# Performance work log

Hardware: AMD Instinct MI355X
Metric: run time of the kernel (lower is better)

## Reference

```python
import jax, jax.numpy as jnp
import numpy as np

B, S, H, V = 256, 64, 512, 32000


def setup_inputs() -> dict:
    key = jax.random.key(0)
    ks = jax.random.split(key, 26)
    f32 = jnp.float32

    def n(k, shape, scale):
        return jax.random.normal(k, shape, dtype=f32) * scale

    s_h = 1.0 / np.sqrt(H)        # torch LSTMCell init scale ~ U(-1/sqrt(H),1/sqrt(H)); use normal of same scale
    s_2h = 1.0 / np.sqrt(2 * H)
    kn_h = np.sqrt(2.0 / H)       # kaiming_normal std for (B,H) tensor (fan_in = H)
    kn_2h = np.sqrt(2.0 / (2 * H))

    inp = {}
    inp["x"] = jax.random.randint(ks[0], (B, S), 0, V)
    inp["W_emb"] = n(ks[1], (V, H), 1.0)
    # forward cell
    inp["Wih_f"] = n(ks[2], (4 * H, H), s_h)
    inp["Whh_f"] = n(ks[3], (4 * H, H), s_h)
    inp["bih_f"] = n(ks[4], (4 * H,), s_h)
    inp["bhh_f"] = n(ks[5], (4 * H,), s_h)
    # backward cell
    inp["Wih_b"] = n(ks[6], (4 * H, H), s_h)
    inp["Whh_b"] = n(ks[7], (4 * H, H), s_h)
    inp["bih_b"] = n(ks[8], (4 * H,), s_h)
    inp["bhh_b"] = n(ks[9], (4 * H,), s_h)
    # combiner cell (input 2H, hidden 2H)
    inp["Wih_c"] = n(ks[10], (8 * H, 2 * H), s_2h)
    inp["Whh_c"] = n(ks[11], (8 * H, 2 * H), s_2h)
    inp["bih_c"] = n(ks[12], (8 * H,), s_2h)
    inp["bhh_c"] = n(ks[13], (8 * H,), s_2h)
    # linear head
    inp["Wout"] = n(ks[14], (V, 2 * H), s_2h)
    inp["bout"] = n(ks[15], (V,), s_2h)
    # kaiming-normal initial states
    inp["h0f"] = n(ks[16], (B, H), kn_h)
    inp["c0f"] = n(ks[17], (B, H), kn_h)
    inp["h0b"] = n(ks[18], (B, H), kn_h)
    inp["c0b"] = n(ks[19], (B, H), kn_h)
    inp["h0c"] = n(ks[20], (B, 2 * H), kn_2h)
    inp["c0c"] = n(ks[21], (B, 2 * H), kn_2h)
    return inp


def run_lstm(xs, h0, c0, Wih, Whh, b):
    # xs: (S, B, D). PyTorch LSTMCell gate order: i, f, g, o.
    def step(carry, x_t):
        h, c = carry
        g = x_t @ Wih.T + h @ Whh.T + b
        i, f, gg, o = jnp.split(g, 4, axis=-1)
        i = jax.nn.sigmoid(i)
        f = jax.nn.sigmoid(f)
        gg = jnp.tanh(gg)
        o = jax.nn.sigmoid(o)
        c2 = f * c + i * gg
        h2 = o * jnp.tanh(c2)
        return (h2, c2), h2
    _, hs = jax.lax.scan(step, (h0, c0), xs)
    return hs  # (S, B, hidden)


def reference(x, W_emb, Wih_f, Whh_f, bih_f, bhh_f, Wih_b, Whh_b, bih_b, bhh_b,
              Wih_c, Whh_c, bih_c, bhh_c, Wout, bout, h0f, c0f, h0b, c0b, h0c, c0c):
    b_sz, s_len = x.shape
    W = W_emb.at[0].set(0.0)                 # padding_idx=0
    emb = W[x]                               # (B, S, H)
    seq = emb.reshape(s_len, b_sz, -1)       # faithful to original .view(S, B, -1) (raw reshape, not transpose)
    hf = run_lstm(seq, h0f, c0f, Wih_f, Whh_f, bih_f + bhh_f)            # (S, B, H)
    hb = run_lstm(seq[::-1], h0b, c0b, Wih_b, Whh_b, bih_b + bhh_b)      # (S, B, H), produced order
    comb_in = jnp.concatenate([hf, hb], axis=-1)                          # (S, B, 2H)
    hc = run_lstm(comb_in, h0c, c0c, Wih_c, Whh_c, bih_c + bhh_c)        # (S, B, 2H)
    return hc[-1] @ Wout.T + bout                                         # (B, V)
```

## Files before the change

kernel.cpp:

```cpp
#include <hip/hip_runtime.h>

#define BB 256
#define SS 64
#define HH 512
#define VV 32000

typedef unsigned short u16;
typedef __attribute__((ext_vector_type(8))) short bf16x8;
typedef __attribute__((ext_vector_type(4))) float f32x4;

__device__ __forceinline__ float sigm(float x) { return 1.0f / (1.0f + __expf(-x)); }
__device__ __forceinline__ float tanh_fast(float x) { return 1.0f - 2.0f / (__expf(2.0f * x) + 1.0f); }
__device__ __forceinline__ u16 f2bf(float f) {
    unsigned u = __float_as_uint(f);
    return (u16)((u + 0x7fffu + ((u >> 16) & 1u)) >> 16);
}
__device__ __forceinline__ bf16x8 ld_cvt8(const float* s) {
    float4 v0 = *(const float4*)s, v1 = *(const float4*)(s + 4);
    bf16x8 b;
    b[0] = (short)f2bf(v0.x); b[1] = (short)f2bf(v0.y);
    b[2] = (short)f2bf(v0.z); b[3] = (short)f2bf(v0.w);
    b[4] = (short)f2bf(v1.x); b[5] = (short)f2bf(v1.y);
    b[6] = (short)f2bf(v1.z); b[7] = (short)f2bf(v1.w);
    return b;
}

#define MFMA(a, b, c) __builtin_amdgcn_mfma_f32_16x16x32_bf16(a, b, c, 0, 0, 0)

__global__ __launch_bounds__(256)
void pack_k(const int* __restrict__ x, const float* __restrict__ W_emb,
            const float* __restrict__ Wih_f, const float* __restrict__ Whh_f,
            const float* __restrict__ Wih_b, const float* __restrict__ Whh_b,
            const float* __restrict__ Wih_c, const float* __restrict__ Whh_c,
            u16* __restrict__ Xfrag, u16* __restrict__ Wfsw,
            u16* __restrict__ Wbsw, u16* __restrict__ Wcsw)
{
    const int lane = threadIdx.x & 63;
    const int l15 = lane & 15, quad = lane >> 4;
    const int gw0 = blockIdx.x * 4 + (threadIdx.x >> 6);
    const int nw = gridDim.x * 4;
    for (int task = gw0; task < 40960; task += nw) {
        const float* src; u16* dst; float scale = 1.f;
        if (task < 16384) {
            int s = task >> 8, rem = task & 255, mt = rem >> 4, kc = rem & 15;
            int b = mt * 16 + l15;
            int tok = x[s * 256 + b];
            scale = (tok == 0) ? 0.f : 1.f;
            src = W_emb + (size_t)tok * 512 + kc * 32 + quad * 8;
            dst = Xfrag + ((size_t)(s * 16 + mt) * 16 + kc) * 512 + (size_t)lane * 8;
        } else if (task < 24576) {
            int e = task - 16384;
            int which = e >> 12; e &= 4095;
            int ut = e >> 7, rem = e & 127, kc = rem >> 2, g = rem & 3;
            int row = g * 512 + ut * 16 + l15;
            int k0 = kc * 32 + quad * 8;
            const float* Wih = which ? Wih_b : Wih_f;
            const float* Whh = which ? Whh_b : Whh_f;
            src = (k0 < 512) ? (Wih + (size_t)row * 512 + k0)
                             : (Whh + (size_t)row * 512 + (k0 - 512));
            u16* W = which ? Wbsw : Wfsw;
            dst = W + ((size_t)(ut * 32 + kc) * 4 + g) * 512 + (size_t)lane * 8;
        } else {
            int e = task - 24576;
            int ut = e >> 8, rem = e & 255, kc = rem >> 2, g = rem & 3;
            int row = g * 1024 + ut * 16 + l15;
            int k0 = kc * 32 + quad * 8;
            src = (k0 < 1024) ? (Wih_c + (size_t)row * 1024 + k0)
                              : (Whh_c + (size_t)row * 1024 + (k0 - 1024));
            dst = Wcsw + ((size_t)(ut * 64 + kc) * 4 + g) * 512 + (size_t)lane * 8;
        }
        float4 v0 = *(const float4*)src;
        float4 v1 = *(const float4*)(src + 4);
        bf16x8 o;
        o[0] = (short)f2bf(v0.x * scale); o[1] = (short)f2bf(v0.y * scale);
        o[2] = (short)f2bf(v0.z * scale); o[3] = (short)f2bf(v0.w * scale);
        o[4] = (short)f2bf(v1.x * scale); o[5] = (short)f2bf(v1.y * scale);
        o[6] = (short)f2bf(v1.z * scale); o[7] = (short)f2bf(v1.w * scale);
        *(bf16x8*)dst = o;
    }
}

__global__ __launch_bounds__(256)
void init_k(const float* __restrict__ bih_f, const float* __restrict__ bhh_f,
            const float* __restrict__ bih_b, const float* __restrict__ bhh_b,
            const float* __restrict__ bih_c, const float* __restrict__ bhh_c,
            const float* __restrict__ h0f, const float* __restrict__ c0f,
            const float* __restrict__ h0b, const float* __restrict__ c0b,
            const float* __restrict__ h0c, const float* __restrict__ c0c,
            float* __restrict__ bsf, float* __restrict__ bsb, float* __restrict__ bsc,
            u16* __restrict__ hf0, u16* __restrict__ hb0, u16* __restrict__ hc0,
            float* __restrict__ cf, float* __restrict__ cb, float* __restrict__ cc)
{
    const int gid = blockIdx.x * 256 + threadIdx.x;
    if (gid < 2048)       bsf[gid] = bih_f[gid] + bhh_f[gid];
    else if (gid < 4096)  { int e = gid - 2048; bsb[e] = bih_b[e] + bhh_b[e]; }
    else if (gid < 8192)  { int e = gid - 4096; bsc[e] = bih_c[e] + bhh_c[e]; }
    const int stride = gridDim.x * 256;
    for (int i = gid; i < 131072; i += stride) {
        int b = i >> 9, k = i & 511;
        int dst = ((b >> 4) * 16 + (k >> 5)) * 512 + (((b & 15) + (((k >> 3) & 3) << 4)) << 3) + (k & 7);
        hf0[dst] = f2bf(h0f[i]);
        hb0[dst] = f2bf(h0b[i]);
        cf[i] = c0f[i];
        cb[i] = c0b[i];
    }
    for (int i = gid; i < 262144; i += stride) {
        int b = i >> 10, k = i & 1023;
        int dst = ((b >> 4) * 32 + (k >> 5)) * 512 + (((b & 15) + (((k >> 3) & 3) << 4)) << 3) + (k & 7);
        hc0[dst] = f2bf(h0c[i]);
        cc[i] = c0c[i];
    }
}

__global__ __launch_bounds__(256)
void step_k(const u16* __restrict__ Xfrag,
            const u16* __restrict__ Wfsw, const u16* __restrict__ Wbsw,
            const u16* __restrict__ Wcsw,
            const float* __restrict__ bsf, const float* __restrict__ bsb,
            const float* __restrict__ bsc,
            const u16* __restrict__ hf_r, u16* __restrict__ hf_w, float* __restrict__ cf,
            const u16* __restrict__ hb_r, u16* __restrict__ hb_w, float* __restrict__ cb,
            const u16* __restrict__ hc_r, u16* __restrict__ hc_w, float* __restrict__ cc,
            int t)
{
    __shared__ __align__(16) u16 Bsh[2][2][4][512];
    const int tid = threadIdx.x;
    const int w = tid >> 6, lane = tid & 63;
    const int l15 = lane & 15, quad = lane >> 4;
    const int xcd = blockIdx.x & 7, slot = blockIdx.x >> 3;
    const f32x4 z = {0.f, 0.f, 0.f, 0.f};

    if (slot < 32) {
        if (t >= SS) return;
        const int cell = xcd >> 2;
        const int ut = (xcd & 3) * 8 + (slot >> 2);
        const int mq = slot & 3;
        const int mt = mq * 4 + w;
        const u16* Wsw = cell ? Wbsw : Wfsw;
        const float* bs = cell ? bsb : bsf;
        const u16* h_r = cell ? hb_r : hf_r;
        u16* h_w = cell ? hb_w : hf_w;
        float* c = cell ? cb : cf;
        const int s2 = cell ? (SS - 1 - t) : t;

        const u16* wstage = Wsw + (size_t)ut * 65536 + (size_t)w * 512 + (size_t)lane * 8;
        const u16* xb0 = Xfrag + ((size_t)(s2 * 16 + mt) * 16) * 512 + (size_t)lane * 8;
        const u16* hp0 = h_r + ((size_t)(mt * 16)) * 512 + (size_t)lane * 8;

        f32x4 acc[4];
#pragma unroll
        for (int g = 0; g < 4; ++g) acc[g] = z;

#define AFB(f) (((f) < 16) ? (xb0 + (size_t)(f) * 512) : (hp0 + (size_t)((f) - 16) * 512))
        bf16x8 a0[3], a1[3];
        {
            bf16x8 w00 = *(const bf16x8*)(wstage);
            bf16x8 w01 = *(const bf16x8*)(wstage + 2048);
            bf16x8 w10 = *(const bf16x8*)(wstage + 2 * 2048);
            bf16x8 w11 = *(const bf16x8*)(wstage + 3 * 2048);
            a0[0] = *(const bf16x8*)AFB(0); a1[0] = *(const bf16x8*)AFB(1);
            a0[1] = *(const bf16x8*)AFB(2); a1[1] = *(const bf16x8*)AFB(3);
            *(bf16x8*)&Bsh[0][0][w][(size_t)lane * 8] = w00;
            *(bf16x8*)&Bsh[0][1][w][(size_t)lane * 8] = w01;
            *(bf16x8*)&Bsh[1][0][w][(size_t)lane * 8] = w10;
            *(bf16x8*)&Bsh[1][1][w][(size_t)lane * 8] = w11;
            __syncthreads();
        }
#pragma unroll
        for (int p = 0; p < 16; ++p) {
            const int s = p % 3, sn = (p + 2) % 3, cur = p & 1;
            bf16x8 wr0, wr1;
            const bool pre = (p + 2 < 16);
            if (pre) {
                wr0 = *(const bf16x8*)(wstage + (size_t)(2 * p + 4) * 2048);
                wr1 = *(const bf16x8*)(wstage + (size_t)(2 * p + 5) * 2048);
                a0[sn] = *(const bf16x8*)AFB(2 * p + 4);
                a1[sn] = *(const bf16x8*)AFB(2 * p + 5);
            }
#pragma unroll
            for (int g = 0; g < 4; ++g) {
                bf16x8 b0 = *(const bf16x8*)&Bsh[cur][0][g][(size_t)lane * 8];
                bf16x8 b1 = *(const bf16x8*)&Bsh[cur][1][g][(size_t)lane * 8];
                acc[g] = MFMA(a0[s], b0, acc[g]);
                acc[g] = MFMA(a1[s], b1, acc[g]);
            }
            __syncthreads();
            if (pre) {
                *(bf16x8*)&Bsh[cur][0][w][(size_t)lane * 8] = wr0;
                *(bf16x8*)&Bsh[cur][1][w][(size_t)lane * 8] = wr1;
            }
        }
#undef AFB

        const int u = ut * 16 + l15;
        const float bi_ = bs[u], bf_ = bs[512 + u], bg_ = bs[1024 + u], bo_ = bs[1536 + u];
        const int fragk = ut >> 1;
        const int lanehi = ((ut & 1) * 2 + (l15 >> 3)) << 4;
        const int j = l15 & 7;
#pragma unroll
        for (int r = 0; r < 4; ++r) {
            const int b = mt * 16 + quad * 4 + r;
            const size_t ci = (size_t)b * 512 + u;
            float i_ = sigm(acc[0][r] + bi_);
            float f_ = sigm(acc[1][r] + bf_);
            float g_ = tanh_fast(acc[2][r] + bg_);
            float o_ = sigm(acc[3][r] + bo_);
            float c2 = f_ * c[ci] + i_ * g_;
            c[ci] = c2;
            h_w[(size_t)(mt * 16 + fragk) * 512 + (size_t)((quad * 4 + r) + lanehi) * 8 + j]
                = f2bf(o_ * tanh_fast(c2));
        }
    } else {
        if (t == 0) return;
        const int cs = slot - 32;
        const int ut = xcd * 8 + (cs >> 2);
        const int mq = cs & 3;
        const int mt = mq * 4 + w;

        const u16* wstage = Wcsw + (size_t)ut * 131072 + (size_t)w * 512 + (size_t)lane * 8;
        const u16* hfa = hf_r + ((size_t)(mt * 16)) * 512 + (size_t)lane * 8;
        const u16* hba = hb_r + ((size_t)(mt * 16)) * 512 + (size_t)lane * 8;
        const u16* hca = hc_r + ((size_t)(mt * 32)) * 512 + (size_t)lane * 8;

        f32x4 acc[4];
#pragma unroll
        for (int g = 0; g < 4; ++g) acc[g] = z;

#define ACB(f)  (((f) < 16) ? (hfa + (size_t)(f) * 512) \
               : ((f) < 32) ? (hba + (size_t)((f) - 16) * 512) \
                            : (hca + (size_t)((f) - 32) * 512))
        bf16x8 a0[3], a1[3];
        {
            bf16x8 w00 = *(const bf16x8*)(wstage);
            bf16x8 w01 = *(const bf16x8*)(wstage + 2048);
            bf16x8 w10 = *(const bf16x8*)(wstage + 2 * 2048);
            bf16x8 w11 = *(const bf16x8*)(wstage + 3 * 2048);
            a0[0] = *(const bf16x8*)ACB(0); a1[0] = *(const bf16x8*)ACB(1);
            a0[1] = *(const bf16x8*)ACB(2); a1[1] = *(const bf16x8*)ACB(3);
            *(bf16x8*)&Bsh[0][0][w][(size_t)lane * 8] = w00;
            *(bf16x8*)&Bsh[0][1][w][(size_t)lane * 8] = w01;
            *(bf16x8*)&Bsh[1][0][w][(size_t)lane * 8] = w10;
            *(bf16x8*)&Bsh[1][1][w][(size_t)lane * 8] = w11;
            __syncthreads();
        }
#pragma unroll
        for (int p = 0; p < 32; ++p) {
            const int s = p % 3, sn = (p + 2) % 3, cur = p & 1;
            bf16x8 wr0, wr1;
            const bool pre = (p + 2 < 32);
            if (pre) {
                wr0 = *(const bf16x8*)(wstage + (size_t)(2 * p + 4) * 2048);
                wr1 = *(const bf16x8*)(wstage + (size_t)(2 * p + 5) * 2048);
                a0[sn] = *(const bf16x8*)ACB(2 * p + 4);
                a1[sn] = *(const bf16x8*)ACB(2 * p + 5);
            }
#pragma unroll
            for (int g = 0; g < 4; ++g) {
                bf16x8 b0 = *(const bf16x8*)&Bsh[cur][0][g][(size_t)lane * 8];
                bf16x8 b1 = *(const bf16x8*)&Bsh[cur][1][g][(size_t)lane * 8];
                acc[g] = MFMA(a0[s], b0, acc[g]);
                acc[g] = MFMA(a1[s], b1, acc[g]);
            }
            __syncthreads();
            if (pre) {
                *(bf16x8*)&Bsh[cur][0][w][(size_t)lane * 8] = wr0;
                *(bf16x8*)&Bsh[cur][1][w][(size_t)lane * 8] = wr1;
            }
        }
#undef ACB

        const int u = ut * 16 + l15;
        const float bi_ = bsc[u], bf_ = bsc[1024 + u], bg_ = bsc[2048 + u], bo_ = bsc[3072 + u];
        const int fragk = ut >> 1;
        const int lanehi = ((ut & 1) * 2 + (l15 >> 3)) << 4;
        const int j = l15 & 7;
#pragma unroll
        for (int r = 0; r < 4; ++r) {
            const int b = mt * 16 + quad * 4 + r;
            const size_t ci = (size_t)b * 1024 + u;
            float i_ = sigm(acc[0][r] + bi_);
            float f_ = sigm(acc[1][r] + bf_);
            float g_ = tanh_fast(acc[2][r] + bg_);
            float o_ = sigm(acc[3][r] + bo_);
            float c2 = f_ * cc[ci] + i_ * g_;
            cc[ci] = c2;
            hc_w[(size_t)(mt * 32 + fragk) * 512 + (size_t)((quad * 4 + r) + lanehi) * 8 + j]
                = f2bf(o_ * tanh_fast(c2));
        }
    }
}

__global__ __launch_bounds__(256)
void head_v3(const u16* __restrict__ A,
             const float* __restrict__ W,
             const float* __restrict__ bias,
             float* __restrict__ out)
{
    __shared__ __align__(16) u16 Bsh[2][2][4][512];
    const int tid = threadIdx.x;
    const int w = tid >> 6, lane = tid & 63;
    const int l15 = lane & 15, quad = lane >> 4;
    const int bid = blockIdx.x;
    const int ntw = bid * 4 + w;

    const float* wsrc = W + (size_t)(ntw * 16 + l15) * 1024 + (size_t)quad * 8;
    const u16* ha[4];
#pragma unroll
    for (int mi = 0; mi < 4; ++mi)
        ha[mi] = A + ((size_t)((w * 4 + mi) * 32)) * 512 + (size_t)lane * 8;

    f32x4 acc[4][4];
#pragma unroll
    for (int mi = 0; mi < 4; ++mi)
#pragma unroll
        for (int nt = 0; nt < 4; ++nt) acc[mi][nt] = {0.f, 0.f, 0.f, 0.f};

    {
        bf16x8 s0 = ld_cvt8(wsrc);
        bf16x8 s1 = ld_cvt8(wsrc + 32);
        *(bf16x8*)&Bsh[0][0][w][(size_t)lane * 8] = s0;
        *(bf16x8*)&Bsh[0][1][w][(size_t)lane * 8] = s1;
        __syncthreads();
    }
    for (int p = 0; p < 16; ++p) {
        const int cur = p & 1, nxt = cur ^ 1;
        bf16x8 sa, sb;
        const bool pre = (p + 1 < 16);
        if (pre) {
            sa = ld_cvt8(wsrc + (size_t)(2 * p + 2) * 32);
            sb = ld_cvt8(wsrc + (size_t)(2 * p + 3) * 32);
        }
        bf16x8 a0[4], a1[4];
#pragma unroll
        for (int mi = 0; mi < 4; ++mi) {
            a0[mi] = *(const bf16x8*)(ha[mi] + (size_t)(2 * p) * 512);
            a1[mi] = *(const bf16x8*)(ha[mi] + (size_t)(2 * p + 1) * 512);
        }
#pragma unroll
        for (int nt = 0; nt < 4; ++nt) {
            bf16x8 b0 = *(const bf16x8*)&Bsh[cur][0][nt][(size_t)lane * 8];
            bf16x8 b1 = *(const bf16x8*)&Bsh[cur][1][nt][(size_t)lane * 8];
#pragma unroll
            for (int mi = 0; mi < 4; ++mi) {
                acc[mi][nt] = MFMA(a0[mi], b0, acc[mi][nt]);
                acc[mi][nt] = MFMA(a1[mi], b1, acc[mi][nt]);
            }
        }
        if (pre) {
            *(bf16x8*)&Bsh[nxt][0][w][(size_t)lane * 8] = sa;
            *(bf16x8*)&Bsh[nxt][1][w][(size_t)lane * 8] = sb;
        }
        __syncthreads();
    }

#pragma unroll
    for (int nt = 0; nt < 4; ++nt) {
        const int n = (bid * 4 + nt) * 16 + l15;
        const float bv = bias[n];
#pragma unroll
        for (int mi = 0; mi < 4; ++mi) {
            const int mt = w * 4 + mi;
#pragma unroll
            for (int r = 0; r < 4; ++r)
                out[(size_t)(mt * 16 + quad * 4 + r) * VV + n] = acc[mi][nt][r] + bv;
        }
    }
}

extern "C" void kernel_launch(void* const* d_in, const int* in_sizes, int n_in,
                              void* d_out, int out_size, void* d_ws, size_t ws_size,
                              hipStream_t stream) {
    const int*   x     = (const int*)d_in[0];
    const float* W_emb = (const float*)d_in[1];
    const float* Wih_f = (const float*)d_in[2];
    const float* Whh_f = (const float*)d_in[3];
    const float* bih_f = (const float*)d_in[4];
    const float* bhh_f = (const float*)d_in[5];
    const float* Wih_b = (const float*)d_in[6];
    const float* Whh_b = (const float*)d_in[7];
    const float* bih_b = (const float*)d_in[8];
    const float* bhh_b = (const float*)d_in[9];
    const float* Wih_c = (const float*)d_in[10];
    const float* Whh_c = (const float*)d_in[11];
    const float* bih_c = (const float*)d_in[12];
    const float* bhh_c = (const float*)d_in[13];
    const float* Wout  = (const float*)d_in[14];
    const float* bout  = (const float*)d_in[15];
    const float* h0f   = (const float*)d_in[16];
    const float* c0f   = (const float*)d_in[17];
    const float* h0b   = (const float*)d_in[18];
    const float* c0b   = (const float*)d_in[19];
    const float* h0c   = (const float*)d_in[20];
    const float* c0c   = (const float*)d_in[21];

    char* p = (char*)d_ws;
    u16* Wfsw = (u16*)p; p += (size_t)2048 * 1024 * 2;
    u16* Wbsw = (u16*)p; p += (size_t)2048 * 1024 * 2;
    u16* Wcsw = (u16*)p; p += (size_t)4096 * 2048 * 2;
    u16* Xfrag = (u16*)p; p += (size_t)8388608 * 2;
    float* bsf = (float*)p; p += 2048 * 4;
    float* bsb = (float*)p; p += 2048 * 4;
    float* bsc = (float*)p; p += 4096 * 4;
    u16* hf[2]; hf[0] = (u16*)p; p += 131072 * 2; hf[1] = (u16*)p; p += 131072 * 2;
    u16* hb[2]; hb[0] = (u16*)p; p += 131072 * 2; hb[1] = (u16*)p; p += 131072 * 2;
    u16* hc[2]; hc[0] = (u16*)p; p += 262144 * 2; hc[1] = (u16*)p; p += 262144 * 2;
    float* cf = (float*)p; p += 131072 * 4;
    float* cb = (float*)p; p += 131072 * 4;
    float* cc = (float*)p; p += 262144 * 4;

    pack_k<<<dim3(2560), dim3(256), 0, stream>>>(
        x, W_emb, Wih_f, Whh_f, Wih_b, Whh_b, Wih_c, Whh_c,
        Xfrag, Wfsw, Wbsw, Wcsw);
    init_k<<<dim3(1024), dim3(256), 0, stream>>>(
        bih_f, bhh_f, bih_b, bhh_b, bih_c, bhh_c,
        h0f, c0f, h0b, c0b, h0c, c0c,
        bsf, bsb, bsc, hf[0], hb[0], hc[0], cf, cb, cc);

    for (int t = 0; t <= SS; ++t) {
        step_k<<<dim3(512), dim3(256), 0, stream>>>(
            Xfrag, Wfsw, Wbsw, Wcsw, bsf, bsb, bsc,
            hf[t & 1], hf[(t + 1) & 1], cf,
            hb[t & 1], hb[(t + 1) & 1], cb,
            hc[(t + 1) & 1], hc[t & 1], cc, t);
    }
    head_v3<<<dim3(500), dim3(256), 0, stream>>>(hc[0], Wout, bout, (float*)d_out);
}
```

Baseline: 1.185 ms.

## Split recurrent-step K dimension across warp pairs with LDS reduction

Each step block's four warps now work as two K-halves times two M-tile pairs instead of four independent M tiles. Each warp covers two M tiles over half the K range, which halves the serial pipeline length per step. The partial sums are then exchanged through shared memory and added before the gate nonlinearities. This shortens the per-step critical path of the latency-bound recurrence. In exchange it doubles the LDS weight staging, raises register pressure from twice as many accumulators and A buffers, and adds one barrier plus a reduction.

```diff
diff --git a/kernel.cpp b/kernel.cpp
--- a/kernel.cpp
+++ b/kernel.cpp
@@ -123,19 +123,21 @@
             const u16* __restrict__ hc_r, u16* __restrict__ hc_w, float* __restrict__ cc,
             int t)
 {
-    __shared__ __align__(16) u16 Bsh[2][2][4][512];
+    __shared__ __align__(16) u16 Bsh[2][2][2][4][512];
     const int tid = threadIdx.x;
     const int w = tid >> 6, lane = tid & 63;
     const int l15 = lane & 15, quad = lane >> 4;
     const int xcd = blockIdx.x & 7, slot = blockIdx.x >> 3;
+    const int kh = w >> 1, mi = w & 1;
     const f32x4 z = {0.f, 0.f, 0.f, 0.f};
+    f32x4* Red = (f32x4*)&Bsh[0][0][0][0][0];
 
     if (slot < 32) {
         if (t >= SS) return;
         const int cell = xcd >> 2;
         const int ut = (xcd & 3) * 8 + (slot >> 2);
         const int mq = slot & 3;
-        const int mt = mq * 4 + w;
+        const int mt0 = mq * 4 + 2 * mi;
         const u16* Wsw = cell ? Wbsw : Wfsw;
         const float* bs = cell ? bsb : bsf;
         const u16* h_r = cell ? hb_r : hf_r;
@@ -143,55 +145,90 @@
         float* c = cell ? cb : cf;
         const int s2 = cell ? (SS - 1 - t) : t;
 
-        const u16* wstage = Wsw + (size_t)ut * 65536 + (size_t)w * 512 + (size_t)lane * 8;
-        const u16* xb0 = Xfrag + ((size_t)(s2 * 16 + mt) * 16) * 512 + (size_t)lane * 8;
-        const u16* hp0 = h_r + ((size_t)(mt * 16)) * 512 + (size_t)lane * 8;
-
-        f32x4 acc[4];
-#pragma unroll
-        for (int g = 0; g < 4; ++g) acc[g] = z;
-
-#define AFB(f) (((f) < 16) ? (xb0 + (size_t)(f) * 512) : (hp0 + (size_t)((f) - 16) * 512))
-        bf16x8 a0[3], a1[3];
+        const u16* wb = Wsw + (size_t)ut * 65536 + (size_t)w * 512 + (size_t)lane * 8;
+        const u16* xb0 = Xfrag + ((size_t)(s2 * 16 + mt0) * 16) * 512 + (size_t)lane * 8;
+        const u16* hp0 = h_r + ((size_t)(mt0 * 16)) * 512 + (size_t)lane * 8;
+        const u16* Ab = kh ? hp0 : xb0;
+
+        f32x4 acc[2][4];
+#pragma unroll
+        for (int m2 = 0; m2 < 2; ++m2)
+#pragma unroll
+            for (int g = 0; g < 4; ++g) acc[m2][g] = z;
+
+        bf16x8 aE0[3], aE1[3], aO0[3], aO1[3];
         {
-            bf16x8 w00 = *(const bf16x8*)(wstage);
-            bf16x8 w01 = *(const bf16x8*)(wstage + 2048);
-            bf16x8 w10 = *(const bf16x8*)(wstage + 2 * 2048);
-            bf16x8 w11 = *(const bf16x8*)(wstage + 3 * 2048);
-            a0[0] = *(const bf16x8*)AFB(0); a1[0] = *(const bf16x8*)AFB(1);
-            a0[1] = *(const bf16x8*)AFB(2); a1[1] = *(const bf16x8*)AFB(3);
-            *(bf16x8*)&Bsh[0][0][w][(size_t)lane * 8] = w00;
-            *(bf16x8*)&Bsh[0][1][w][(size_t)lane * 8] = w01;
-            *(bf16x8*)&Bsh[1][0][w][(size_t)lane * 8] = w10;
-            *(bf16x8*)&Bsh[1][1][w][(size_t)lane * 8] = w11;
+            bf16x8 ws0 = *(const bf16x8*)(wb);
+            bf16x8 ws1 = *(const bf16x8*)(wb + 1 * 2048);
+            bf16x8 ws2 = *(const bf16x8*)(wb + 16 * 2048);
+            bf16x8 ws3 = *(const bf16x8*)(wb + 17 * 2048);
+            bf16x8 ws4 = *(const bf16x8*)(wb + 2 * 2048);
+            bf16x8 ws5 = *(const bf16x8*)(wb + 3 * 2048);
+            bf16x8 ws6 = *(const bf16x8*)(wb + 18 * 2048);
+            bf16x8 ws7 = *(const bf16x8*)(wb + 19 * 2048);
+            aE0[0] = *(const bf16x8*)(Ab);
+            aO0[0] = *(const bf16x8*)(Ab + 512);
+            aE1[0] = *(const bf16x8*)(Ab + 8192);
+            aO1[0] = *(const bf16x8*)(Ab + 8192 + 512);
+            aE0[1] = *(const bf16x8*)(Ab + 2 * 512);
+            aO0[1] = *(const bf16x8*)(Ab + 3 * 512);
+            aE1[1] = *(const bf16x8*)(Ab + 8192 + 2 * 512);
+            aO1[1] = *(const bf16x8*)(Ab + 8192 + 3 * 512);
+            *(bf16x8*)&Bsh[0][0][0][w][(size_t)lane * 8] = ws0;
+            *(bf16x8*)&Bsh[0][0][1][w][(size_t)lane * 8] = ws1;
+            *(bf16x8*)&Bsh[0][1][0][w][(size_t)lane * 8] = ws2;
+            *(bf16x8*)&Bsh[0][1][1][w][(size_t)lane * 8] = ws3;
+            *(bf16x8*)&Bsh[1][0][0][w][(size_t)lane * 8] = ws4;
+            *(bf16x8*)&Bsh[1][0][1][w][(size_t)lane * 8] = ws5;
+            *(bf16x8*)&Bsh[1][1][0][w][(size_t)lane * 8] = ws6;
+            *(bf16x8*)&Bsh[1][1][1][w][(size_t)lane * 8] = ws7;
             __syncthreads();
         }
 #pragma unroll
-        for (int p = 0; p < 16; ++p) {
+        for (int p = 0; p < 8; ++p) {
             const int s = p % 3, sn = (p + 2) % 3, cur = p & 1;
-            bf16x8 wr0, wr1;
-            const bool pre = (p + 2 < 16);
+            bf16x8 wr0, wr1, wr2, wr3;
+            const bool pre = (p + 2 < 8);
             if (pre) {
-                wr0 = *(const bf16x8*)(wstage + (size_t)(2 * p + 4) * 2048);
-                wr1 = *(const bf16x8*)(wstage + (size_t)(2 * p + 5) * 2048);
-                a0[sn] = *(const bf16x8*)AFB(2 * p + 4);
-                a1[sn] = *(const bf16x8*)AFB(2 * p + 5);
+                wr0 = *(const bf16x8*)(wb + (size_t)(2 * p + 4) * 2048);
+                wr1 = *(const bf16x8*)(wb + (size_t)(2 * p + 5) * 2048);
+                wr2 = *(const bf16x8*)(wb + (size_t)(20 + 2 * p) * 2048);
+                wr3 = *(const bf16x8*)(wb + (size_t)(21 + 2 * p) * 2048);
+                aE0[sn] = *(const bf16x8*)(Ab + (size_t)(2 * p + 4) * 512);
+                aO0[sn] = *(const bf16x8*)(Ab + (size_t)(2 * p + 5) * 512);
+                aE1[sn] = *(const bf16x8*)(Ab + 8192 + (size_t)(2 * p + 4) * 512);
+                aO1[sn] = *(const bf16x8*)(Ab + 8192 + (size_t)(2 * p + 5) * 512);
             }
 #pragma unroll
             for (int g = 0; g < 4; ++g) {
-                bf16x8 b0 = *(const bf16x8*)&Bsh[cur][0][g][(size_t)lane * 8];
-                bf16x8 b1 = *(const bf16x8*)&Bsh[cur][1][g][(size_t)lane * 8];
-                acc[g] = MFMA(a0[s], b0, acc[g]);
-                acc[g] = MFMA(a1[s], b1, acc[g]);
+                bf16x8 b0 = *(const bf16x8*)&Bsh[cur][kh][0][g][(size_t)lane * 8];
+                bf16x8 b1 = *(const bf16x8*)&Bsh[cur][kh][1][g][(size_t)lane * 8];
+                acc[0][g] = MFMA(aE0[s], b0, acc[0][g]);
+                acc[1][g] = MFMA(aE1[s], b0, acc[1][g]);
+                acc[0][g] = MFMA(aO0[s], b1, acc[0][g]);
+                acc[1][g] = MFMA(aO1[s], b1, acc[1][g]);
             }
             __syncthreads();
             if (pre) {
-                *(bf16x8*)&Bsh[cur][0][w][(size_t)lane * 8] = wr0;
-                *(bf16x8*)&Bsh[cur][1][w][(size_t)lane * 8] = wr1;
-            }
-        }
-#undef AFB
-
+                *(bf16x8*)&Bsh[cur][0][0][w][(size_t)lane * 8] = wr0;
+                *(bf16x8*)&Bsh[cur][0][1][w][(size_t)lane * 8] = wr1;
+                *(bf16x8*)&Bsh[cur][1][0][w][(size_t)lane * 8] = wr2;
+                *(bf16x8*)&Bsh[cur][1][1][w][(size_t)lane * 8] = wr3;
+            }
+        }
+        {
+            const int po = 1 - kh;
+#pragma unroll
+            for (int g = 0; g < 4; ++g)
+                Red[((size_t)w * 64 + lane) * 4 + g] = acc[po][g];
+        }
+        __syncthreads();
+#pragma unroll
+        for (int g = 0; g < 4; ++g) {
+            f32x4 o = Red[((size_t)(w ^ 2) * 64 + lane) * 4 + g];
+            acc[kh][g] += o;
+        }
+        const int mtF = mt0 + kh;
         const int u = ut * 16 + l15;
         const float bi_ = bs[u], bf_ = bs[512 + u], bg_ = bs[1024 + u], bo_ = bs[1536 + u];
         const int fragk = ut >> 1;
@@ -199,15 +236,15 @@
         const int j = l15 & 7;
 #pragma unroll
         for (int r = 0; r < 4; ++r) {
-            const int b = mt * 16 + quad * 4 + r;
+            const int b = mtF * 16 + quad * 4 + r;
             const size_t ci = (size_t)b * 512 + u;
-            float i_ = sigm(acc[0][r] + bi_);
-            float f_ = sigm(acc[1][r] + bf_);
-            float g_ = tanh_fast(acc[2][r] + bg_);
-            float o_ = sigm(acc[3][r] + bo_);
+            float i_ = sigm(acc[kh][0][r] + bi_);
+            float f_ = sigm(acc[kh][1][r] + bf_);
+            float g_ = tanh_fast(acc[kh][2][r] + bg_);
+            float o_ = sigm(acc[kh][3][r] + bo_);
             float c2 = f_ * c[ci] + i_ * g_;
             c[ci] = c2;
-            h_w[(size_t)(mt * 16 + fragk) * 512 + (size_t)((quad * 4 + r) + lanehi) * 8 + j]
+            h_w[(size_t)(mtF * 16 + fragk) * 512 + (size_t)((quad * 4 + r) + lanehi) * 8 + j]
                 = f2bf(o_ * tanh_fast(c2));
         }
     } else {
@@ -215,60 +252,95 @@
         const int cs = slot - 32;
         const int ut = xcd * 8 + (cs >> 2);
         const int mq = cs & 3;
-        const int mt = mq * 4 + w;
-
-        const u16* wstage = Wcsw + (size_t)ut * 131072 + (size_t)w * 512 + (size_t)lane * 8;
-        const u16* hfa = hf_r + ((size_t)(mt * 16)) * 512 + (size_t)lane * 8;
-        const u16* hba = hb_r + ((size_t)(mt * 16)) * 512 + (size_t)lane * 8;
-        const u16* hca = hc_r + ((size_t)(mt * 32)) * 512 + (size_t)lane * 8;
-
-        f32x4 acc[4];
-#pragma unroll
-        for (int g = 0; g < 4; ++g) acc[g] = z;
-
-#define ACB(f)  (((f) < 16) ? (hfa + (size_t)(f) * 512) \
-               : ((f) < 32) ? (hba + (size_t)((f) - 16) * 512) \
-                            : (hca + (size_t)((f) - 32) * 512))
-        bf16x8 a0[3], a1[3];
+        const int mt0 = mq * 4 + 2 * mi;
+
+        const u16* wb = Wcsw + (size_t)ut * 131072 + (size_t)w * 512 + (size_t)lane * 8;
+        const u16* hfa = hf_r + ((size_t)(mt0 * 16)) * 512 + (size_t)lane * 8;
+        const u16* hba = hb_r + ((size_t)(mt0 * 16)) * 512 + (size_t)lane * 8;
+        const u16* hca = hc_r + ((size_t)(mt0 * 32)) * 512 + (size_t)lane * 8;
+        const size_t astr = kh ? 16384 : 8192;
+
+#define AC(f) ((kh) ? (hca + (size_t)(f) * 512) \
+             : (((f) < 16) ? (hfa + (size_t)(f) * 512) : (hba + (size_t)((f) - 16) * 512)))
+
+        f32x4 acc[2][4];
+#pragma unroll
+        for (int m2 = 0; m2 < 2; ++m2)
+#pragma unroll
+            for (int g = 0; g < 4; ++g) acc[m2][g] = z;
+
+        bf16x8 aE0[3], aE1[3], aO0[3], aO1[3];
         {
-            bf16x8 w00 = *(const bf16x8*)(wstage);
-            bf16x8 w01 = *(const bf16x8*)(wstage + 2048);
-            bf16x8 w10 = *(const bf16x8*)(wstage + 2 * 2048);
-            bf16x8 w11 = *(const bf16x8*)(wstage + 3 * 2048);
-            a0[0] = *(const bf16x8*)ACB(0); a1[0] = *(const bf16x8*)ACB(1);
-            a0[1] = *(const bf16x8*)ACB(2); a1[1] = *(const bf16x8*)ACB(3);
-            *(bf16x8*)&Bsh[0][0][w][(size_t)lane * 8] = w00;
-            *(bf16x8*)&Bsh[0][1][w][(size_t)lane * 8] = w01;
-            *(bf16x8*)&Bsh[1][0][w][(size_t)lane * 8] = w10;
-            *(bf16x8*)&Bsh[1][1][w][(size_t)lane * 8] = w11;
+            bf16x8 ws0 = *(const bf16x8*)(wb);
+            bf16x8 ws1 = *(const bf16x8*)(wb + 1 * 2048);
+            bf16x8 ws2 = *(const bf16x8*)(wb + 32 * 2048);
+            bf16x8 ws3 = *(const bf16x8*)(wb + 33 * 2048);
+            bf16x8 ws4 = *(const bf16x8*)(wb + 2 * 2048);
+            bf16x8 ws5 = *(const bf16x8*)(wb + 3 * 2048);
+            bf16x8 ws6 = *(const bf16x8*)(wb + 34 * 2048);
+            bf16x8 ws7 = *(const bf16x8*)(wb + 35 * 2048);
+            const u16* f0 = AC(0); const u16* f1 = AC(1);
+            const u16* f2 = AC(2); const u16* f3 = AC(3);
+            aE0[0] = *(const bf16x8*)f0;          aO0[0] = *(const bf16x8*)f1;
+            aE1[0] = *(const bf16x8*)(f0 + astr); aO1[0] = *(const bf16x8*)(f1 + astr);
+            aE0[1] = *(const bf16x8*)f2;          aO0[1] = *(const bf16x8*)f3;
+            aE1[1] = *(const bf16x8*)(f2 + astr); aO1[1] = *(const bf16x8*)(f3 + astr);
+            *(bf16x8*)&Bsh[0][0][0][w][(size_t)lane * 8] = ws0;
+            *(bf16x8*)&Bsh[0][0][1][w][(size_t)lane * 8] = ws1;
+            *(bf16x8*)&Bsh[0][1][0][w][(size_t)lane * 8] = ws2;
+            *(bf16x8*)&Bsh[0][1][1][w][(size_t)lane * 8] = ws3;
+            *(bf16x8*)&Bsh[1][0][0][w][(size_t)lane * 8] = ws4;
+            *(bf16x8*)&Bsh[1][0][1][w][(size_t)lane * 8] = ws5;
+            *(bf16x8*)&Bsh[1][1][0][w][(size_t)lane * 8] = ws6;
+            *(bf16x8*)&Bsh[1][1][1][w][(size_t)lane * 8] = ws7;
             __syncthreads();
         }
 #pragma unroll
-        for (int p = 0; p < 32; ++p) {
+        for (int p = 0; p < 16; ++p) {
             const int s = p % 3, sn = (p + 2) % 3, cur = p & 1;
-            bf16x8 wr0, wr1;
-            const bool pre = (p + 2 < 32);
+            bf16x8 wr0, wr1, wr2, wr3;
+            const bool pre = (p + 2 < 16);
             if (pre) {
-                wr0 = *(const bf16x8*)(wstage + (size_t)(2 * p + 4) * 2048);
-                wr1 = *(const bf16x8*)(wstage + (size_t)(2 * p + 5) * 2048);
-                a0[sn] = *(const bf16x8*)ACB(2 * p + 4);
-                a1[sn] = *(const bf16x8*)ACB(2 * p + 5);
+                wr0 = *(const bf16x8*)(wb + (size_t)(2 * p + 4) * 2048);
+                wr1 = *(const bf16x8*)(wb + (size_t)(2 * p + 5) * 2048);
+                wr2 = *(const bf16x8*)(wb + (size_t)(36 + 2 * p) * 2048);
+                wr3 = *(const bf16x8*)(wb + (size_t)(37 + 2 * p) * 2048);
+                const u16* f0 = AC(2 * p + 4);
+                const u16* f1 = AC(2 * p + 5);
+                aE0[sn] = *(const bf16x8*)f0;          aO0[sn] = *(const bf16x8*)f1;
+                aE1[sn] = *(const bf16x8*)(f0 + astr); aO1[sn] = *(const bf16x8*)(f1 + astr);
             }
 #pragma unroll
             for (int g = 0; g < 4; ++g) {
-                bf16x8 b0 = *(const bf16x8*)&Bsh[cur][0][g][(size_t)lane * 8];
-                bf16x8 b1 = *(const bf16x8*)&Bsh[cur][1][g][(size_t)lane * 8];
-                acc[g] = MFMA(a0[s], b0, acc[g]);
-                acc[g] = MFMA(a1[s], b1, acc[g]);
+                bf16x8 b0 = *(const bf16x8*)&Bsh[cur][kh][0][g][(size_t)lane * 8];
+                bf16x8 b1 = *(const bf16x8*)&Bsh[cur][kh][1][g][(size_t)lane * 8];
+                acc[0][g] = MFMA(aE0[s], b0, acc[0][g]);
+                acc[1][g] = MFMA(aE1[s], b0, acc[1][g]);
+                acc[0][g] = MFMA(aO0[s], b1, acc[0][g]);
+                acc[1][g] = MFMA(aO1[s], b1, acc[1][g]);
             }
             __syncthreads();
             if (pre) {
-                *(bf16x8*)&Bsh[cur][0][w][(size_t)lane * 8] = wr0;
-                *(bf16x8*)&Bsh[cur][1][w][(size_t)lane * 8] = wr1;
-            }
-        }
-#undef ACB
-
+                *(bf16x8*)&Bsh[cur][0][0][w][(size_t)lane * 8] = wr0;
+                *(bf16x8*)&Bsh[cur][0][1][w][(size_t)lane * 8] = wr1;
+                *(bf16x8*)&Bsh[cur][1][0][w][(size_t)lane * 8] = wr2;
+                *(bf16x8*)&Bsh[cur][1][1][w][(size_t)lane * 8] = wr3;
+            }
+        }
+#undef AC
+        {
+            const int po = 1 - kh;
+#pragma unroll
+            for (int g = 0; g < 4; ++g)
+                Red[((size_t)w * 64 + lane) * 4 + g] = acc[po][g];
+        }
+        __syncthreads();
+#pragma unroll
+        for (int g = 0; g < 4; ++g) {
+            f32x4 o = Red[((size_t)(w ^ 2) * 64 + lane) * 4 + g];
+            acc[kh][g] += o;
+        }
+        const int mtF = mt0 + kh;
         const int u = ut * 16 + l15;
         const float bi_ = bsc[u], bf_ = bsc[1024 + u], bg_ = bsc[2048 + u], bo_ = bsc[3072 + u];
         const int fragk = ut >> 1;
@@ -276,15 +348,15 @@
         const int j = l15 & 7;
 #pragma unroll
         for (int r = 0; r < 4; ++r) {
-            const int b = mt * 16 + quad * 4 + r;
+            const int b = mtF * 16 + quad * 4 + r;
             const size_t ci = (size_t)b * 1024 + u;
-            float i_ = sigm(acc[0][r] + bi_);
-            float f_ = sigm(acc[1][r] + bf_);
-            float g_ = tanh_fast(acc[2][r] + bg_);
-            float o_ = sigm(acc[3][r] + bo_);
+            float i_ = sigm(acc[kh][0][r] + bi_);
+            float f_ = sigm(acc[kh][1][r] + bf_);
+            float g_ = tanh_fast(acc[kh][2][r] + bg_);
+            float o_ = sigm(acc[kh][3][r] + bo_);
             float c2 = f_ * cc[ci] + i_ * g_;
             cc[ci] = c2;
-            hc_w[(size_t)(mt * 32 + fragk) * 512 + (size_t)((quad * 4 + r) + lanehi) * 8 + j]
+            hc_w[(size_t)(mtF * 32 + fragk) * 512 + (size_t)((quad * 4 + r) + lanehi) * 8 + j]
                 = f2bf(o_ * tanh_fast(c2));
         }
     }
```

Result: slower. 1.633 ms (+37.8%).
